# Optimization experiments

Measured on AMD Instinct MI355X. Metric: run time of the kernel, lower is better.

The kernel has to match this reference:

```python
import jax, jax.numpy as jnp
import numpy as np

COMMITMENT_COST = 0.25
NUM_EMBEDDINGS = 1024
EMBEDDING_DIM = 512  # win_size(8) * num_pellets(64)


def setup_inputs() -> dict:
    key = jax.random.key(0)
    k1, k2 = jax.random.split(key)
    inputs = jax.random.normal(k1, (64, 256, EMBEDDING_DIM), dtype=jnp.float32)
    # matches torch init: uniform_(-1/K, 1/K)
    lim = 1.0 / NUM_EMBEDDINGS
    emb_weight = jax.random.uniform(k2, (NUM_EMBEDDINGS, EMBEDDING_DIM),
                                    dtype=jnp.float32, minval=-lim, maxval=lim)
    return {"inputs": inputs, "emb_weight": emb_weight}


def reference(inputs, emb_weight):
    batch_size = inputs.shape[0]
    input_shape = inputs.shape
    flat = inputs.reshape(-1, EMBEDDING_DIM)  # [N, D]

    distances = (jnp.sum(flat * flat, axis=1, keepdims=True)
                 + jnp.sum(emb_weight * emb_weight, axis=1)
                 - 2.0 * flat @ emb_weight.T)
    encoding_indices = jnp.argmin(distances, axis=1)  # [N]

    # gather instead of one-hot matmul (same math)
    quantized = emb_weight[encoding_indices].reshape(input_shape)

    e_latent_loss = jnp.mean((jax.lax.stop_gradient(quantized) - inputs) ** 2)
    q_latent_loss = jnp.mean((quantized - jax.lax.stop_gradient(inputs)) ** 2)
    loss_vq = q_latent_loss + COMMITMENT_COST * e_latent_loss

    # straight-through estimator
    quantized = inputs + jax.lax.stop_gradient(quantized - inputs)

    encoding_indices = encoding_indices.reshape(batch_size, -1)
    return loss_vq, quantized, encoding_indices
```

## Files before the change

### kernel.cpp

```cpp
#include <hip/hip_runtime.h>
#include <cfloat>

#define NROWS  16384
#define DIM    512
#define KC     1024
#define QELEMS (NROWS * DIM)

#define NSPLIT 8
#define CHUNKS 132

typedef float  floatx4 __attribute__((ext_vector_type(4)));
typedef _Float16 half8 __attribute__((ext_vector_type(8)));
typedef _Float16 half4 __attribute__((ext_vector_type(4)));

__global__ __launch_bounds__(256) void prep_kernel(const float* __restrict__ A,
                                                   const float* __restrict__ E,
                                                   float* __restrict__ xsq,
                                                   float* __restrict__ esq,
                                                   _Float16* __restrict__ ah,
                                                   _Float16* __restrict__ al,
                                                   _Float16* __restrict__ eh,
                                                   _Float16* __restrict__ el,
                                                   unsigned long long* __restrict__ packed,
                                                   float* __restrict__ out) {
    if (blockIdx.x == 0 && threadIdx.x == 0) out[0] = 0.f;
    const int wave = threadIdx.x >> 6, lane = threadIdx.x & 63;
    const bool isA = blockIdx.x < (NROWS / 4);
    const int row = (isA ? blockIdx.x : blockIdx.x - NROWS / 4) * 4 + wave;
    const float* M = isA ? A : E;
    const float scale = isA ? 2048.0f : 65536.0f;

    const float4* Mr = (const float4*)(M + (size_t)row * DIM);
    float4 va = Mr[lane];
    float4 vb = Mr[lane + 64];
    float s = 0.f;
    s += va.x*va.x + va.y*va.y + va.z*va.z + va.w*va.w;
    s += vb.x*vb.x + vb.y*vb.y + vb.z*vb.z + vb.w*vb.w;
    #pragma unroll
    for (int off = 32; off; off >>= 1) s += __shfl_down(s, off, 64);
    if (lane == 0) {
        if (isA) { xsq[row] = s; packed[row] = ~0ULL; }
        else     { esq[row] = s; }
    }

    float xa[4] = {va.x, va.y, va.z, va.w}, xb[4] = {vb.x, vb.y, vb.z, vb.w};
    half4 ha, la, hb, lb;
    #pragma unroll
    for (int e = 0; e < 4; ++e) {
        float t = xa[e] * scale;
        _Float16 h = (_Float16)t;
        ha[e] = h; la[e] = (_Float16)(t - (float)h);
        t = xb[e] * scale;
        h = (_Float16)t;
        hb[e] = h; lb[e] = (_Float16)(t - (float)h);
    }
    _Float16* hr = (isA ? ah : eh) + (size_t)row * DIM;
    _Float16* lr = (isA ? al : el) + (size_t)row * DIM;
    ((half4*)hr)[lane]      = ha;
    ((half4*)lr)[lane]      = la;
    ((half4*)hr)[lane + 64] = hb;
    ((half4*)lr)[lane + 64] = lb;
}

__global__ __launch_bounds__(256) void mfma_argmin_kernel(const _Float16* __restrict__ ah,
                                                          const _Float16* __restrict__ al,
                                                          const _Float16* __restrict__ eh,
                                                          const _Float16* __restrict__ el,
                                                          const float* __restrict__ esq,
                                                          const float* __restrict__ xsq,
                                                          unsigned long long* __restrict__ packed) {
    __shared__ half8 AhT[2][4 * CHUNKS], AlT[2][4 * CHUNKS];
    __shared__ half8 EhT[2][4 * CHUNKS], ElT[2][4 * CHUNKS];
    __shared__ float redv[128][2];
    __shared__ int   redi[128][2];

    const int tid = threadIdx.x;
    const int lane = tid & 63, wave = tid >> 6;
    const int wm = wave >> 1, wn = wave & 1;
    const int tx = lane & 15, qd = lane >> 4;
    const int bm = blockIdx.x & 127, bn = blockIdx.x >> 7;
    const int m0 = bm * 128, c0 = bn * 128;

    const int srow = tid >> 2, skq = tid & 3;
    const _Float16* gA  = ah + (size_t)(m0 + srow) * DIM + skq * 8;
    const _Float16* gAl = al + (size_t)(m0 + srow) * DIM + skq * 8;
    const _Float16* gE  = eh + (size_t)(c0 + srow) * DIM + skq * 8;
    const _Float16* gEl = el + (size_t)(c0 + srow) * DIM + skq * 8;
    const int cw0 = skq * CHUNKS + srow, cw1 = cw0 + 64;

    floatx4 acc[4][4];
    #pragma unroll
    for (int i = 0; i < 4; ++i)
        #pragma unroll
        for (int j = 0; j < 4; ++j) acc[i][j] = (floatx4){0.f, 0.f, 0.f, 0.f};

    half8 rA0  = *(const half8*)(gA);
    half8 rA1  = *(const half8*)(gA  + 64 * DIM);
    half8 rL0  = *(const half8*)(gAl);
    half8 rL1  = *(const half8*)(gAl + 64 * DIM);
    half8 rE0  = *(const half8*)(gE);
    half8 rE1  = *(const half8*)(gE  + 64 * DIM);
    half8 rF0  = *(const half8*)(gEl);
    half8 rF1  = *(const half8*)(gEl + 64 * DIM);
    AhT[0][cw0] = rA0; AhT[0][cw1] = rA1;
    AlT[0][cw0] = rL0; AlT[0][cw1] = rL1;
    EhT[0][cw0] = rE0; EhT[0][cw1] = rE1;
    ElT[0][cw0] = rF0; ElT[0][cw1] = rF1;

    #pragma unroll 1
    for (int kt = 0; kt < DIM / 32; ++kt) {
        const int cur = kt & 1, nxt = cur ^ 1;
        const int kb = (kt + 1) * 32;
        if (kt < DIM / 32 - 1) {
            rA0 = *(const half8*)(gA  + kb);
            rA1 = *(const half8*)(gA  + 64 * DIM + kb);
            rL0 = *(const half8*)(gAl + kb);
            rL1 = *(const half8*)(gAl + 64 * DIM + kb);
            rE0 = *(const half8*)(gE  + kb);
            rE1 = *(const half8*)(gE  + 64 * DIM + kb);
            rF0 = *(const half8*)(gEl + kb);
            rF1 = *(const half8*)(gEl + 64 * DIM + kb);
        }
        __syncthreads();

        half8 fa[4], fbh[4], fbl[4];
        #pragma unroll
        for (int i = 0; i < 4; ++i)
            fa[i] = AhT[cur][qd * CHUNKS + wm * 64 + i * 16 + tx];
        #pragma unroll
        for (int j = 0; j < 4; ++j) {
            fbh[j] = EhT[cur][qd * CHUNKS + wn * 64 + j * 16 + tx];
            fbl[j] = ElT[cur][qd * CHUNKS + wn * 64 + j * 16 + tx];
        }
        #pragma unroll
        for (int i = 0; i < 4; ++i)
            #pragma unroll
            for (int j = 0; j < 4; ++j)
                acc[i][j] = __builtin_amdgcn_mfma_f32_16x16x32_f16(fa[i], fbh[j], acc[i][j], 0, 0, 0);
        #pragma unroll
        for (int i = 0; i < 4; ++i)
            #pragma unroll
            for (int j = 0; j < 4; ++j)
                acc[i][j] = __builtin_amdgcn_mfma_f32_16x16x32_f16(fa[i], fbl[j], acc[i][j], 0, 0, 0);
        #pragma unroll
        for (int i = 0; i < 4; ++i)
            fa[i] = AlT[cur][qd * CHUNKS + wm * 64 + i * 16 + tx];
        #pragma unroll
        for (int i = 0; i < 4; ++i)
            #pragma unroll
            for (int j = 0; j < 4; ++j)
                acc[i][j] = __builtin_amdgcn_mfma_f32_16x16x32_f16(fa[i], fbh[j], acc[i][j], 0, 0, 0);

        if (kt < DIM / 32 - 1) {
            AhT[nxt][cw0] = rA0; AhT[nxt][cw1] = rA1;
            AlT[nxt][cw0] = rL0; AlT[nxt][cw1] = rL1;
            EhT[nxt][cw0] = rE0; EhT[nxt][cw1] = rE1;
            ElT[nxt][cw0] = rF0; ElT[nxt][cw1] = rF1;
        }
    }

    float sqe_v[4];
    #pragma unroll
    for (int j = 0; j < 4; ++j) sqe_v[j] = esq[c0 + wn * 64 + j * 16 + tx];
    #pragma unroll
    for (int i = 0; i < 4; ++i) {
        #pragma unroll
        for (int r = 0; r < 4; ++r) {
            int rl = wm * 64 + i * 16 + qd * 4 + r;
            float sx = xsq[m0 + rl];
            float bvv = FLT_MAX; int bii = 0x7fffffff;
            #pragma unroll
            for (int j = 0; j < 4; ++j) {
                float S = sx + sqe_v[j];
                float s = S - acc[i][j][r] * (1.0f / 67108864.0f);
                int c = c0 + wn * 64 + j * 16 + tx;
                if (s < bvv || (s == bvv && c < bii)) { bvv = s; bii = c; }
            }
            #pragma unroll
            for (int md = 1; md < 16; md <<= 1) {
                float ov = __shfl_xor(bvv, md, 64);
                int   oc = __shfl_xor(bii, md, 64);
                if (ov < bvv || (ov == bvv && oc < bii)) { bvv = ov; bii = oc; }
            }
            if (tx == 0) { redv[rl][wn] = bvv; redi[rl][wn] = bii; }
        }
    }
    __syncthreads();
    if (tid < 128) {
        float v0 = redv[tid][0], v1 = redv[tid][1];
        int   i0 = redi[tid][0], i1 = redi[tid][1];
        float v = (v1 < v0) ? v1 : v0;
        int   ix = (v1 < v0) ? i1 : i0;
        unsigned long long pk = ((unsigned long long)__float_as_uint(v) << 32)
                              | (unsigned int)ix;
        atomicMin(&packed[m0 + tid], pk);
    }
}

__global__ __launch_bounds__(256) void finalize_kernel(const float* __restrict__ E,
                                                       const unsigned long long* __restrict__ packed,
                                                       float* __restrict__ out) {
    float* q = out + 1;
    float* idxF = out + 1 + QELEMS;
    const int tid = threadIdx.x;
    const int r0 = blockIdx.x * 64;

    __shared__ int sidx[64];
    if (tid < 64) {
        unsigned long long pk = packed[r0 + tid];
        int idx = (int)(unsigned int)(pk & 0xFFFFFFFFull);
        float sc = __uint_as_float((unsigned int)(pk >> 32));
        sidx[tid] = idx;
        idxF[r0 + tid] = (float)idx;
        #pragma unroll
        for (int off = 32; off; off >>= 1) sc += __shfl_down(sc, off, 64);
        if (tid == 0) atomicAdd(out, sc * (1.25f / (float)QELEMS));
    }
    __syncthreads();

    #pragma unroll 4
    for (int it = 0; it < 32; ++it) {
        int flat = it * 256 + tid;
        int row = flat >> 7;
        int d4  = (flat & 127) * 4;
        int idx = sidx[row];
        float4 e = *(const float4*)(E + (size_t)idx * DIM + d4);
        *(float4*)(q + (size_t)(r0 + row) * DIM + d4) = e;
    }
}

extern "C" void kernel_launch(void* const* d_in, const int* in_sizes, int n_in,
                              void* d_out, int out_size, void* d_ws, size_t ws_size,
                              hipStream_t stream) {
    const float* A = (const float*)d_in[0];
    const float* E = (const float*)d_in[1];
    float* out = (float*)d_out;

    unsigned long long* packed = (unsigned long long*)d_ws;
    float*    esq  = (float*)(packed + NROWS);
    float*    xsq  = esq + KC;
    _Float16* eh   = (_Float16*)(xsq + NROWS);
    _Float16* el   = eh + (size_t)KC * DIM;
    _Float16* ah   = el + (size_t)KC * DIM;
    _Float16* al   = ah + (size_t)NROWS * DIM;

    prep_kernel<<<NROWS / 4 + KC / 4, 256, 0, stream>>>(A, E, xsq, esq, ah, al, eh, el, packed, out);
    mfma_argmin_kernel<<<(NROWS / 128) * NSPLIT, 256, 0, stream>>>(
        ah, al, eh, el, esq, xsq, packed);
    finalize_kernel<<<NROWS / 64, 256, 0, stream>>>(E, packed, out);
}
```

Baseline: 174.0 us.

## Load codebook fragments directly from global memory, shrink LDS, raise occupancy

The MFMA argmin kernel stops staging codebook (E) hi/lo tiles in shared memory. Each wave now loads its B fragments straight from global or L2 into registers every k-step, which halves LDS use and removes the E LDS writes and reads. The LDS row padding changes from 132 to 130 and launch bounds now request 3 blocks per CU to raise occupancy. The finalize kernel uses smaller blocks of 16 rows for more parallelism. In exchange, global loads are no longer coalesced across the tile and every wave re-reads E from L2, and the occupancy hint may cause register spilling.

Result: slower. 187.6 us (+7.8%).

```diff
diff --git a/kernel.cpp b/kernel.cpp
--- a/kernel.cpp
+++ b/kernel.cpp
@@ -7,7 +7,7 @@
 #define QELEMS (NROWS * DIM)
 
 #define NSPLIT 8
-#define CHUNKS 132
+#define CHUNKS 130
 
 typedef float  floatx4 __attribute__((ext_vector_type(4)));
 typedef _Float16 half8 __attribute__((ext_vector_type(8)));
@@ -62,15 +62,14 @@
     ((half4*)lr)[lane + 64] = lb;
 }
 
-__global__ __launch_bounds__(256) void mfma_argmin_kernel(const _Float16* __restrict__ ah,
-                                                          const _Float16* __restrict__ al,
-                                                          const _Float16* __restrict__ eh,
-                                                          const _Float16* __restrict__ el,
-                                                          const float* __restrict__ esq,
-                                                          const float* __restrict__ xsq,
-                                                          unsigned long long* __restrict__ packed) {
+__global__ __launch_bounds__(256, 3) void mfma_argmin_kernel(const _Float16* __restrict__ ah,
+                                                             const _Float16* __restrict__ al,
+                                                             const _Float16* __restrict__ eh,
+                                                             const _Float16* __restrict__ el,
+                                                             const float* __restrict__ esq,
+                                                             const float* __restrict__ xsq,
+                                                             unsigned long long* __restrict__ packed) {
     __shared__ half8 AhT[2][4 * CHUNKS], AlT[2][4 * CHUNKS];
-    __shared__ half8 EhT[2][4 * CHUNKS], ElT[2][4 * CHUNKS];
     __shared__ float redv[128][2];
     __shared__ int   redi[128][2];
 
@@ -84,54 +83,49 @@
     const int srow = tid >> 2, skq = tid & 3;
     const _Float16* gA  = ah + (size_t)(m0 + srow) * DIM + skq * 8;
     const _Float16* gAl = al + (size_t)(m0 + srow) * DIM + skq * 8;
-    const _Float16* gE  = eh + (size_t)(c0 + srow) * DIM + skq * 8;
-    const _Float16* gEl = el + (size_t)(c0 + srow) * DIM + skq * 8;
     const int cw0 = skq * CHUNKS + srow, cw1 = cw0 + 64;
 
+    const _Float16* gBh = eh + (size_t)(c0 + wn * 64 + tx) * DIM + qd * 8;
+    const _Float16* gBl = el + (size_t)(c0 + wn * 64 + tx) * DIM + qd * 8;
+
     floatx4 acc[4][4];
     #pragma unroll
     for (int i = 0; i < 4; ++i)
         #pragma unroll
         for (int j = 0; j < 4; ++j) acc[i][j] = (floatx4){0.f, 0.f, 0.f, 0.f};
 
-    half8 rA0  = *(const half8*)(gA);
-    half8 rA1  = *(const half8*)(gA  + 64 * DIM);
-    half8 rL0  = *(const half8*)(gAl);
-    half8 rL1  = *(const half8*)(gAl + 64 * DIM);
-    half8 rE0  = *(const half8*)(gE);
-    half8 rE1  = *(const half8*)(gE  + 64 * DIM);
-    half8 rF0  = *(const half8*)(gEl);
-    half8 rF1  = *(const half8*)(gEl + 64 * DIM);
+    half8 rA0 = *(const half8*)(gA);
+    half8 rA1 = *(const half8*)(gA  + 64 * DIM);
+    half8 rL0 = *(const half8*)(gAl);
+    half8 rL1 = *(const half8*)(gAl + 64 * DIM);
     AhT[0][cw0] = rA0; AhT[0][cw1] = rA1;
     AlT[0][cw0] = rL0; AlT[0][cw1] = rL1;
-    EhT[0][cw0] = rE0; EhT[0][cw1] = rE1;
-    ElT[0][cw0] = rF0; ElT[0][cw1] = rF1;
 
     #pragma unroll 1
     for (int kt = 0; kt < DIM / 32; ++kt) {
         const int cur = kt & 1, nxt = cur ^ 1;
         const int kb = (kt + 1) * 32;
+        const int ke = kt * 32;
+
+        half8 fbh[4], fbl[4];
+        #pragma unroll
+        for (int j = 0; j < 4; ++j)
+            fbh[j] = *(const half8*)(gBh + (size_t)j * 16 * DIM + ke);
         if (kt < DIM / 32 - 1) {
             rA0 = *(const half8*)(gA  + kb);
             rA1 = *(const half8*)(gA  + 64 * DIM + kb);
             rL0 = *(const half8*)(gAl + kb);
             rL1 = *(const half8*)(gAl + 64 * DIM + kb);
-            rE0 = *(const half8*)(gE  + kb);
-            rE1 = *(const half8*)(gE  + 64 * DIM + kb);
-            rF0 = *(const half8*)(gEl + kb);
-            rF1 = *(const half8*)(gEl + 64 * DIM + kb);
-        }
+        }
+        #pragma unroll
+        for (int j = 0; j < 4; ++j)
+            fbl[j] = *(const half8*)(gBl + (size_t)j * 16 * DIM + ke);
         __syncthreads();
 
-        half8 fa[4], fbh[4], fbl[4];
+        half8 fa[4];
         #pragma unroll
         for (int i = 0; i < 4; ++i)
             fa[i] = AhT[cur][qd * CHUNKS + wm * 64 + i * 16 + tx];
-        #pragma unroll
-        for (int j = 0; j < 4; ++j) {
-            fbh[j] = EhT[cur][qd * CHUNKS + wn * 64 + j * 16 + tx];
-            fbl[j] = ElT[cur][qd * CHUNKS + wn * 64 + j * 16 + tx];
-        }
         #pragma unroll
         for (int i = 0; i < 4; ++i)
             #pragma unroll
@@ -154,8 +148,6 @@
         if (kt < DIM / 32 - 1) {
             AhT[nxt][cw0] = rA0; AhT[nxt][cw1] = rA1;
             AlT[nxt][cw0] = rL0; AlT[nxt][cw1] = rL1;
-            EhT[nxt][cw0] = rE0; EhT[nxt][cw1] = rE1;
-            ElT[nxt][cw0] = rF0; ElT[nxt][cw1] = rF1;
         }
     }
 
@@ -203,23 +195,26 @@
     float* q = out + 1;
     float* idxF = out + 1 + QELEMS;
     const int tid = threadIdx.x;
-    const int r0 = blockIdx.x * 64;
-
-    __shared__ int sidx[64];
+    const int r0 = blockIdx.x * 16;
+
+    __shared__ int sidx[16];
     if (tid < 64) {
-        unsigned long long pk = packed[r0 + tid];
-        int idx = (int)(unsigned int)(pk & 0xFFFFFFFFull);
-        float sc = __uint_as_float((unsigned int)(pk >> 32));
-        sidx[tid] = idx;
-        idxF[r0 + tid] = (float)idx;
-        #pragma unroll
-        for (int off = 32; off; off >>= 1) sc += __shfl_down(sc, off, 64);
+        float sc = 0.f;
+        if (tid < 16) {
+            unsigned long long pk = packed[r0 + tid];
+            int idx = (int)(unsigned int)(pk & 0xFFFFFFFFull);
+            sc = __uint_as_float((unsigned int)(pk >> 32));
+            sidx[tid] = idx;
+            idxF[r0 + tid] = (float)idx;
+        }
+        #pragma unroll
+        for (int off = 8; off; off >>= 1) sc += __shfl_down(sc, off, 16);
         if (tid == 0) atomicAdd(out, sc * (1.25f / (float)QELEMS));
     }
     __syncthreads();
 
     #pragma unroll 4
-    for (int it = 0; it < 32; ++it) {
+    for (int it = 0; it < 8; ++it) {
         int flat = it * 256 + tid;
         int row = flat >> 7;
         int d4  = (flat & 127) * 4;
@@ -247,5 +242,5 @@
     prep_kernel<<<NROWS / 4 + KC / 4, 256, 0, stream>>>(A, E, xsq, esq, ah, al, eh, el, packed, out);
     mfma_argmin_kernel<<<(NROWS / 128) * NSPLIT, 256, 0, stream>>>(
         ah, al, eh, el, esq, xsq, packed);
-    finalize_kernel<<<NROWS / 64, 256, 0, stream>>>(E, packed, out);
-}
+    finalize_kernel<<<NROWS / 16, 256, 0, stream>>>(E, packed, out);
+}
```
